# Kernel optimization log

Hardware: AMD Instinct MI355X
Metric: run time of the kernel (lower is better)

Reference implementation:

```python
import jax, jax.numpy as jnp
import numpy as np

N = 100000      # nodes (accounts)
E = 500000      # edges (transactions)
F_NODE = 128
F_EDGE = 32
HEADS = 4
C = 64          # hidden_channels per head
HC = HEADS * C  # 256
OUT = 32
BN_EPS = 1e-5
NEG_SLOPE = 0.2


def setup_inputs() -> dict:
    key = jax.random.key(0)
    ks = jax.random.split(key, 24)
    rn = lambda k, shape, s=0.05: (jax.random.normal(k, shape, jnp.float32) * s)
    inp = {
        "x": jax.random.normal(ks[0], (N, F_NODE), jnp.float32),
        "edge_index": jax.random.randint(ks[1], (2, E), 0, N, dtype=jnp.int32),
        "edge_attr": jax.random.normal(ks[2], (E, F_EDGE), jnp.float32),
        # node_proj
        "Wp": rn(ks[3], (F_NODE, C)), "bp": jnp.zeros((C,), jnp.float32),
    }
    in_dims = [C, HC, HC]
    i = 4
    for l, d in enumerate(in_dims):
        inp[f"Wg{l}"] = rn(ks[i], (d, HC)); i += 1
        inp[f"as{l}"] = rn(ks[i], (HEADS, C)); i += 1
        inp[f"ad{l}"] = rn(ks[i], (HEADS, C)); i += 1
        inp[f"bg{l}"] = jnp.zeros((HC,), jnp.float32)
        inp[f"g{l}"] = jnp.ones((HC,), jnp.float32)   # BN gamma
        inp[f"be{l}"] = jnp.zeros((HC,), jnp.float32)  # BN beta
    inp["W1"] = rn(ks[i], (2 * HC + F_EDGE, OUT)); inp["b1"] = jnp.zeros((OUT,), jnp.float32)
    inp["W2"] = rn(ks[i + 1], (OUT, 1)); inp["b2"] = jnp.zeros((1,), jnp.float32)
    return inp


def _gat_layer(h, src, dst, Wg, att_s, att_d, bg):
    # PyG GATConv (concat=True, add_self_loops=False), eval mode (no dropout).
    xh = (h @ Wg).reshape(N, HEADS, C)                      # [N,H,C]
    a_s = jnp.sum(xh * att_s, axis=-1)                      # [N,H]
    a_d = jnp.sum(xh * att_d, axis=-1)                      # [N,H]
    e = jax.nn.leaky_relu(a_s[src] + a_d[dst], NEG_SLOPE)   # [E,H]
    m = jax.lax.stop_gradient(jax.ops.segment_max(e, dst, num_segments=N))
    ex = jnp.exp(e - m[dst])
    den = jax.ops.segment_sum(ex, dst, num_segments=N)      # [N,H]
    alpha = ex / (den[dst] + 1e-16)                         # softmax over in-edges of dst
    agg = jax.ops.segment_sum(xh[src] * alpha[:, :, None], dst, num_segments=N)
    return agg.reshape(N, HC) + bg


def _forward(x, edge_index, edge_attr, Wp, bp,
             Wg0, as0, ad0, bg0, g0, be0,
             Wg1, as1, ad1, bg1, g1, be1,
             Wg2, as2, ad2, bg2, g2, be2,
             W1, b1, W2, b2):
    src, dst = edge_index[0], edge_index[1]
    h = jax.nn.relu(x @ Wp + bp)                            # [N,64]
    bn_scale = 1.0 / jnp.sqrt(jnp.float32(1.0) + BN_EPS)    # BN eval: mean=0, var=1
    layers = [(Wg0, as0, ad0, bg0, g0, be0),
              (Wg1, as1, ad1, bg1, g1, be1),
              (Wg2, as2, ad2, bg2, g2, be2)]
    for Wg, a_s, a_d, bg, g, be in layers:
        hn = _gat_layer(h, src, dst, Wg, a_s, a_d, bg)
        hn = jax.nn.relu(hn * (g * bn_scale) + be)          # BatchNorm(eval) + ReLU
        h = h + hn if h.shape == hn.shape else hn           # residual (skipped at layer 0)
    # decode_edges: MLP(src_emb || dst_emb || edge_attr) without materializing the concat:
    W1s, W1d, W1e = W1[:HC], W1[HC:2 * HC], W1[2 * HC:]
    z = jax.nn.relu((h @ W1s)[src] + (h @ W1d)[dst] + edge_attr @ W1e + b1)  # [E,32]
    return (z @ W2 + b2)[:, 0]                              # [E] fraud logits


def reference(x, edge_index, edge_attr, Wp, bp,
              Wg0, as0, ad0, bg0, g0, be0,
              Wg1, as1, ad1, bg1, g1, be1,
              Wg2, as2, ad2, bg2, g2, be2,
              W1, b1, W2, b2):
    return _forward(x, edge_index, edge_attr, Wp, bp,
                    Wg0, as0, ad0, bg0, g0, be0,
                    Wg1, as1, ad1, bg1, g1, be1,
                    Wg2, as2, ad2, bg2, g2, be2,
                    W1, b1, W2, b2)
```

## Files before the change

### kernel.cpp

```cpp
#include <hip/hip_runtime.h>
#include <hip/hip_fp16.h>

#define NN 100000
#define EE 500000
#define F_NODE 128
#define F_EDGE 32
#define HEADS 4
#define CC 64
#define HC 256
#define OUTD 32
#define NEG_SLOPE 0.2f
#define BN_SCALE 0.9999950000374997f
#define NB_SCAN 391
#define MPAD 100096

using half8 = __attribute__((ext_vector_type(8))) _Float16;
using f32x4 = __attribute__((ext_vector_type(4))) float;

typedef const __attribute__((address_space(1))) void* gas_ptr;
typedef __attribute__((address_space(3))) void* las_ptr;

template<int K, int NOUT, int MODE, int ATT>
__global__ __launch_bounds__(256, 2) void mgemm2(const __half* __restrict__ A,
                                                 const __half* __restrict__ Wt,
                                                 const float* __restrict__ bias,
                                                 __half* __restrict__ C,
                                                 const float* __restrict__ as_,
                                                 const float* __restrict__ ad_,
                                                 float* __restrict__ a_s,
                                                 float* __restrict__ a_d) {
    constexpr int BM = 128;
    constexpr int BN = (NOUT >= 128) ? 128 : 64;
    constexpr int MI = 4;
    constexpr int NI = BN / 32;
    constexpr int KS = K / 64;
    constexpr int ABYTES = BM * 128;
    constexpr int BBYTES = BN * 128;
    __shared__ char smem[2 * (ABYTES + BBYTES)];

    const int tid  = threadIdx.x;
    const int wave = tid >> 6, lane = tid & 63;
    const int wr = wave >> 1, wc = wave & 1;
    const int lrow = lane & 15, kq = lane >> 4;
    const int m0 = blockIdx.x * BM;
    const int n0 = blockIdx.y * BN;
    const int srow = tid >> 3;
    const int sunit = tid & 7;
    const int wofs = (tid & 192) * 16;

    auto stage = [&](int buf, int ks) {
        char* base = smem + buf * (ABYTES + BBYTES);
        const int kk = ks * 64;
#pragma unroll
        for (int it = 0; it < BM / 32; ++it) {
            const int r = srow + it * 32;
            const __half* src = A + (size_t)(m0 + r) * K + kk + ((sunit ^ (r & 7)) << 3);
            __builtin_amdgcn_global_load_lds((gas_ptr)src,
                (las_ptr)(base + it * 4096 + wofs), 16, 0, 0);
        }
#pragma unroll
        for (int it = 0; it < BN / 32; ++it) {
            const int r = srow + it * 32;
            const __half* src = Wt + (size_t)(n0 + r) * K + kk + ((sunit ^ (r & 7)) << 3);
            __builtin_amdgcn_global_load_lds((gas_ptr)src,
                (las_ptr)(base + ABYTES + it * 4096 + wofs), 16, 0, 0);
        }
    };

    f32x4 acc[MI][NI] = {};

    auto compute = [&](int buf) {
        const char* Ab = smem + buf * (ABYTES + BBYTES);
        const char* Bb = Ab + ABYTES;
#pragma unroll
        for (int k32 = 0; k32 < 2; ++k32) {
            const int ku = k32 * 4 + kq;
            half8 af[MI], bf[NI];
#pragma unroll
            for (int mi = 0; mi < MI; ++mi) {
                const int rr = wr * 64 + mi * 16 + lrow;
                af[mi] = *(const half8*)(Ab + rr * 128 + ((ku ^ (rr & 7)) << 4));
            }
#pragma unroll
            for (int ni = 0; ni < NI; ++ni) {
                const int rc = wc * (BN / 2) + ni * 16 + lrow;
                bf[ni] = *(const half8*)(Bb + rc * 128 + ((ku ^ (rc & 7)) << 4));
            }
#pragma unroll
            for (int mi = 0; mi < MI; ++mi)
#pragma unroll
                for (int ni = 0; ni < NI; ++ni)
                    acc[mi][ni] = __builtin_amdgcn_mfma_f32_16x16x32_f16(
                        af[mi], bf[ni], acc[mi][ni], 0, 0, 0);
        }
    };

    stage(0, 0);
    __syncthreads();
    int cur = 0;
#pragma unroll
    for (int ks = 0; ks < KS; ++ks) {
        if (ks + 1 < KS) stage(cur ^ 1, ks + 1);
        compute(cur);
        __syncthreads();
        cur ^= 1;
    }

    const int crow = kq * 4;
#pragma unroll
    for (int mi = 0; mi < MI; ++mi) {
#pragma unroll
        for (int ni = 0; ni < NI; ++ni) {
            const int col = n0 + wc * (BN / 2) + ni * 16 + lrow;
            float bcol = (MODE == 1) ? bias[col] : 0.f;
#pragma unroll
            for (int r = 0; r < 4; ++r) {
                float v = acc[mi][ni][r];
                if constexpr (MODE == 1) v = fmaxf(v + bcol, 0.f);
                const int row = m0 + wr * 64 + mi * 16 + crow + r;
                C[(size_t)row * NOUT + col] = __float2half(v);
            }
        }
    }

    if constexpr (ATT) {
        const int head = (n0 + wc * 64) >> 6;
        float wsv[NI], wdv[NI];
#pragma unroll
        for (int ni = 0; ni < NI; ++ni) {
            const int col = n0 + wc * (BN / 2) + ni * 16 + lrow;
            wsv[ni] = as_[col];
            wdv[ni] = ad_[col];
        }
#pragma unroll
        for (int mi = 0; mi < MI; ++mi) {
#pragma unroll
            for (int r = 0; r < 4; ++r) {
                float ss = 0.f, dd = 0.f;
#pragma unroll
                for (int ni = 0; ni < NI; ++ni) {
                    ss += acc[mi][ni][r] * wsv[ni];
                    dd += acc[mi][ni][r] * wdv[ni];
                }
#pragma unroll
                for (int off = 8; off >= 1; off >>= 1) {
                    ss += __shfl_xor(ss, off, 64);
                    dd += __shfl_xor(dd, off, 64);
                }
                if (lrow == 0) {
                    const int row = m0 + wr * 64 + mi * 16 + crow + r;
                    a_s[row * HEADS + head] = ss;
                    a_d[row * HEADS + head] = dd;
                }
            }
        }
    }
}

__global__ __launch_bounds__(256) void wt_conv(const float* __restrict__ W,
                                               __half* __restrict__ Wt,
                                               int K, int N) {
    int idx = blockIdx.x * 256 + threadIdx.x;
    if (idx >= K * N) return;
    int n = idx / K, k = idx % K;
    Wt[idx] = __float2half(W[k * N + n]);
}

__global__ __launch_bounds__(256) void wt_final(const float* __restrict__ W1,
                                                __half* __restrict__ Wt) {
    int idx = blockIdx.x * 256 + threadIdx.x;
    if (idx >= 64 * 256) return;
    int n = idx >> 8, k = idx & 255;
    float v = (n < 32) ? W1[k * 32 + n] : W1[(256 + k) * 32 + (n - 32)];
    Wt[idx] = __float2half(v);
}

__global__ __launch_bounds__(256) void cvt_x(const float* __restrict__ x,
                                             __half* __restrict__ x16) {
    int i = blockIdx.x * 256 + threadIdx.x;
    float4 v = ((const float4*)x)[i];
    __half2* o = (__half2*)x16 + (size_t)i * 2;
    o[0] = __floats2half2_rn(v.x, v.y);
    o[1] = __floats2half2_rn(v.z, v.w);
}

__global__ __launch_bounds__(256) void csr_count(const int* __restrict__ dst,
                                                 int* __restrict__ deg,
                                                 int* __restrict__ pos) {
    int e = blockIdx.x * 256 + threadIdx.x;
    if (e >= EE) return;
    pos[e] = atomicAdd(deg + dst[e], 1);
}

__device__ __forceinline__ int wave_incl_scan(int v, int lane) {
#pragma unroll
    for (int off = 1; off < 64; off <<= 1) {
        int t = __shfl_up(v, off, 64);
        if (lane >= off) v += t;
    }
    return v;
}

__global__ __launch_bounds__(256) void scan1(const int* __restrict__ deg,
                                             int* __restrict__ rowptr,
                                             int* __restrict__ bsum) {
    int tid = threadIdx.x, n = blockIdx.x * 256 + tid;
    int lane = tid & 63, wave = tid >> 6;
    int d = (n < NN) ? deg[n] : 0;
    int v = wave_incl_scan(d, lane);
    __shared__ int ws[4];
    if (lane == 63) ws[wave] = v;
    __syncthreads();
    int woff = 0;
    for (int w = 0; w < wave; ++w) woff += ws[w];
    int incl = v + woff;
    if (n < NN) rowptr[n] = incl - d;
    if (tid == 255) bsum[blockIdx.x] = incl;
}

__global__ __launch_bounds__(512) void scan2(const int* __restrict__ bsum,
                                             int* __restrict__ boff) {
    int t = threadIdx.x;
    int lane = t & 63, wave = t >> 6;
    int d = (t < NB_SCAN) ? bsum[t] : 0;
    int v = wave_incl_scan(d, lane);
    __shared__ int ws[8];
    if (lane == 63) ws[wave] = v;
    __syncthreads();
    int woff = 0;
    for (int w = 0; w < wave; ++w) woff += ws[w];
    if (t < NB_SCAN) boff[t] = v + woff - d;
}

__global__ __launch_bounds__(256) void scan3(int* __restrict__ rowptr,
                                             const int* __restrict__ boff) {
    int n = blockIdx.x * 256 + threadIdx.x;
    if (n == 0) rowptr[NN] = EE;
    if (n < NN) rowptr[n] += boff[blockIdx.x];
}

__global__ __launch_bounds__(256) void csr_scatter(const int* __restrict__ src,
                                                   const int* __restrict__ dst,
                                                   const int* __restrict__ rowptr,
                                                   const int* __restrict__ pos,
                                                   int* __restrict__ srcs) {
    int e = blockIdx.x * 256 + threadIdx.x;
    if (e >= EE) return;
    srcs[rowptr[dst[e]] + pos[e]] = src[e];
}

__global__ __launch_bounds__(256) void gather_agg(const int* __restrict__ rowptr,
                                                  const int* __restrict__ srcs,
                                                  const float* __restrict__ a_s,
                                                  const float* __restrict__ a_d,
                                                  const __half* __restrict__ xh,
                                                  const float* __restrict__ bg,
                                                  const float* __restrict__ g,
                                                  const float* __restrict__ be,
                                                  __half* __restrict__ h,
                                                  int residual) {
    const int n = blockIdx.x * 4 + (threadIdx.x >> 6);
    const int lane = threadIdx.x & 63;
    if (n >= NN) return;
    const int hl = lane >> 5;
    const int l5 = lane & 31;
    const int hd = l5 >> 3;
    const int c0 = l5 * 8;

    const int start = rowptr[n], end = rowptr[n + 1];
    const float adv = a_d[n * HEADS + hd];

    float acc[8] = {};
    float den = 0.f;

    for (int i = start + hl; i < end; i += 8) {
        int  j0 = i,                 j1 = (i + 2 < end) ? i + 2 : i;
        int  j2 = (i + 4 < end) ? i + 4 : i;
        int  j3 = (i + 6 < end) ? i + 6 : i;
        const int s0 = srcs[j0], s1 = srcs[j1], s2 = srcs[j2], s3 = srcs[j3];

        float v0 = a_s[s0 * HEADS + hd] + adv;
        float v1 = a_s[s1 * HEADS + hd] + adv;
        float v2 = a_s[s2 * HEADS + hd] + adv;
        float v3 = a_s[s3 * HEADS + hd] + adv;
        v0 = fmaxf(v0, v0 * NEG_SLOPE);
        v1 = fmaxf(v1, v1 * NEG_SLOPE);
        v2 = fmaxf(v2, v2 * NEG_SLOPE);
        v3 = fmaxf(v3, v3 * NEG_SLOPE);
        float e0 = __expf(v0);
        float e1 = (i + 2 < end) ? __expf(v1) : 0.f;
        float e2 = (i + 4 < end) ? __expf(v2) : 0.f;
        float e3 = (i + 6 < end) ? __expf(v3) : 0.f;

        half8 r0 = *(const half8*)(xh + (size_t)s0 * HC + c0);
        half8 r1 = *(const half8*)(xh + (size_t)s1 * HC + c0);
        half8 r2 = *(const half8*)(xh + (size_t)s2 * HC + c0);
        half8 r3 = *(const half8*)(xh + (size_t)s3 * HC + c0);

#pragma unroll
        for (int k = 0; k < 8; ++k)
            acc[k] += e0 * (float)r0[k] + e1 * (float)r1[k]
                    + e2 * (float)r2[k] + e3 * (float)r3[k];
        den += e0 + e1 + e2 + e3;
    }

    den += __shfl_xor(den, 32, 64);
#pragma unroll
    for (int k = 0; k < 8; ++k) acc[k] += __shfl_xor(acc[k], 32, 64);

    if (hl != 0) return;
    const float inv = 1.f / (den + 1e-16f);

    float bgv[8], gv[8], bev[8];
    *(float4*)(bgv)     = *(const float4*)(bg + c0);
    *(float4*)(bgv + 4) = *(const float4*)(bg + c0 + 4);
    *(float4*)(gv)      = *(const float4*)(g + c0);
    *(float4*)(gv + 4)  = *(const float4*)(g + c0 + 4);
    *(float4*)(bev)     = *(const float4*)(be + c0);
    *(float4*)(bev + 4) = *(const float4*)(be + c0 + 4);

    half8* hp = (half8*)(h + (size_t)n * HC + c0);
    float r[8];
#pragma unroll
    for (int k = 0; k < 8; ++k)
        r[k] = fmaxf((acc[k] * inv + bgv[k]) * (gv[k] * BN_SCALE) + bev[k], 0.f);
    if (residual) {
        half8 old = *hp;
#pragma unroll
        for (int k = 0; k < 8; ++k) r[k] += (float)old[k];
    }
    half8 o;
#pragma unroll
    for (int k = 0; k < 8; ++k) o[k] = (_Float16)r[k];
    __builtin_nontemporal_store(o, hp);
}

__global__ __launch_bounds__(256) void edge_final(const float* __restrict__ ea,
                                                  const __half* __restrict__ w1et,
                                                  const float* __restrict__ b1,
                                                  const int* __restrict__ src,
                                                  const int* __restrict__ dst,
                                                  const __half* __restrict__ hshd,
                                                  const float* __restrict__ W2,
                                                  const float* __restrict__ b2,
                                                  float* __restrict__ out) {
    __shared__ float zl[64][36];
    const int wave = threadIdx.x >> 6, lane = threadIdx.x & 63;
    const int e0 = blockIdx.x * 64;
    const int lrow = lane & 15, kofs = (lane >> 4) * 8;

    int er = e0 + wave * 16 + lrow;
    if (er >= EE) er = EE - 1;
    const float* ap = ea + (size_t)er * F_EDGE + kofs;
    float4 f0 = *(const float4*)ap;
    float4 f1 = *(const float4*)(ap + 4);
    half8 a;
    a[0] = (_Float16)f0.x; a[1] = (_Float16)f0.y;
    a[2] = (_Float16)f0.z; a[3] = (_Float16)f0.w;
    a[4] = (_Float16)f1.x; a[5] = (_Float16)f1.y;
    a[6] = (_Float16)f1.z; a[7] = (_Float16)f1.w;

    half8 b0 = *(const half8*)(w1et + (size_t)lrow * 32 + kofs);
    half8 b1v = *(const half8*)(w1et + (size_t)(16 + lrow) * 32 + kofs);
    f32x4 acc0 = {}, acc1 = {};
    acc0 = __builtin_amdgcn_mfma_f32_16x16x32_f16(a, b0,  acc0, 0, 0, 0);
    acc1 = __builtin_amdgcn_mfma_f32_16x16x32_f16(a, b1v, acc1, 0, 0, 0);

    const int crow = (lane >> 4) * 4;
    const float bc0 = b1[lrow], bc1 = b1[16 + lrow];
#pragma unroll
    for (int r = 0; r < 4; ++r) {
        zl[wave * 16 + crow + r][lrow]      = acc0[r] + bc0;
        zl[wave * 16 + crow + r][16 + lrow] = acc1[r] + bc1;
    }
    __syncthreads();

    const int el = threadIdx.x >> 2, j0 = (threadIdx.x & 3) * 8;
    const int e = e0 + el;
    const bool ok = e < EE;
    const int s = ok ? src[e] : 0;
    const int d = ok ? dst[e] : 0;

    half8 hs = *(const half8*)(hshd + (size_t)s * 64 + j0);
    half8 hdv = *(const half8*)(hshd + (size_t)d * 64 + 32 + j0);
    float w2v[8];
    *(float4*)(w2v)     = *(const float4*)(W2 + j0);
    *(float4*)(w2v + 4) = *(const float4*)(W2 + j0 + 4);
    float4 z0 = *(const float4*)&zl[el][j0];
    float4 z1 = *(const float4*)&zl[el][j0 + 4];

    float acc = 0.f;
    const float* zp0 = &z0.x;
    const float* zp1 = &z1.x;
#pragma unroll
    for (int i = 0; i < 4; ++i) {
        float z = zp0[i] + (float)hs[i] + (float)hdv[i];
        acc += fmaxf(z, 0.f) * w2v[i];
    }
#pragma unroll
    for (int i = 0; i < 4; ++i) {
        float z = zp1[i] + (float)hs[4 + i] + (float)hdv[4 + i];
        acc += fmaxf(z, 0.f) * w2v[4 + i];
    }
    acc += __shfl_xor(acc, 1, 64);
    acc += __shfl_xor(acc, 2, 64);
    if (ok && (threadIdx.x & 3) == 0) out[e] = acc + b2[0];
}

extern "C" void kernel_launch(void* const* d_in, const int* in_sizes, int n_in,
                              void* d_out, int out_size, void* d_ws, size_t ws_size,
                              hipStream_t stream) {
    const float* x  = (const float*)d_in[0];
    const int*   ei = (const int*)d_in[1];
    const float* ea = (const float*)d_in[2];
    const float* Wp = (const float*)d_in[3];
    const float* bp = (const float*)d_in[4];
    const float* W1 = (const float*)d_in[23];
    const float* b1 = (const float*)d_in[24];
    const float* W2 = (const float*)d_in[25];
    const float* b2 = (const float*)d_in[26];
    const int* src = ei;
    const int* dst = ei + EE;

    float* ws = (float*)d_ws;
    __half* h      = (__half*)(ws);
    __half* xh     = (__half*)(ws + 12820000);
    __half* x16    = (__half*)(ws + 25640000);
    __half* h0     = (__half*)(ws + 32050000);
    __half* hshd   = (__half*)(ws + 35260000);
    float*  a_s    = ws + 38470000;
    float*  a_d    = ws + 38880000;
    int*    rowptr = (int*)(ws + 41270000);
    int*    deg    = (int*)(ws + 41380000);
    int*    pos    = (int*)(ws + 41480000);
    int*    srcs   = (int*)(ws + 42490000);
    int*    bsum   = (int*)(ws + 42990000);
    int*    boff   = (int*)(ws + 42991000);
    __half* wpt    = (__half*)(ws + 42992000);
    __half* wgt    = (__half*)(ws + 43000000);
    __half* w1t    = (__half*)(ws + 43020000);
    float*  out    = (float*)d_out;

    const int MB = MPAD / 128;

    hipMemsetAsync(deg, 0, (size_t)NN * sizeof(int), stream);
    csr_count<<<(EE + 255) / 256, 256, 0, stream>>>(dst, deg, pos);
    scan1<<<NB_SCAN, 256, 0, stream>>>(deg, rowptr, bsum);
    scan2<<<1, 512, 0, stream>>>(bsum, boff);
    scan3<<<NB_SCAN, 256, 0, stream>>>(rowptr, boff);
    csr_scatter<<<(EE + 255) / 256, 256, 0, stream>>>(src, dst, rowptr, pos, srcs);

    cvt_x<<<NN * F_NODE / 4 / 256, 256, 0, stream>>>(x, x16);
    wt_conv<<<(F_NODE * 64 + 255) / 256, 256, 0, stream>>>(Wp, wpt, F_NODE, 64);

    mgemm2<F_NODE, 64, 1, 0><<<dim3(MB, 1), 256, 0, stream>>>(
        x16, wpt, bp, h0, nullptr, nullptr, nullptr, nullptr);

    for (int l = 0; l < 3; ++l) {
        const float* Wg  = (const float*)d_in[5 + 6 * l];
        const float* as_ = (const float*)d_in[6 + 6 * l];
        const float* ad_ = (const float*)d_in[7 + 6 * l];
        const float* bg  = (const float*)d_in[8 + 6 * l];
        const float* g   = (const float*)d_in[9 + 6 * l];
        const float* be  = (const float*)d_in[10 + 6 * l];

        if (l == 0) {
            wt_conv<<<(CC * HC + 255) / 256, 256, 0, stream>>>(Wg, wgt, CC, HC);
            mgemm2<CC, HC, 0, 1><<<dim3(MB, 2), 256, 0, stream>>>(
                h0, wgt, nullptr, xh, as_, ad_, a_s, a_d);
        } else {
            wt_conv<<<(HC * HC + 255) / 256, 256, 0, stream>>>(Wg, wgt, HC, HC);
            mgemm2<HC, HC, 0, 1><<<dim3(MB, 2), 256, 0, stream>>>(
                h, wgt, nullptr, xh, as_, ad_, a_s, a_d);
        }

        gather_agg<<<(NN + 3) / 4, 256, 0, stream>>>(rowptr, srcs, a_s, a_d, xh,
                                                     bg, g, be, h, l > 0 ? 1 : 0);
    }

    wt_final<<<(64 * 256 + 255) / 256, 256, 0, stream>>>(W1, w1t);
    mgemm2<HC, 64, 0, 0><<<dim3(MB, 1), 256, 0, stream>>>(
        h, w1t, nullptr, hshd, nullptr, nullptr, nullptr, nullptr);

    wt_conv<<<(32 * 32 + 255) / 256, 256, 0, stream>>>(W1 + 2 * HC * OUTD, wpt, 32, 32);
    edge_final<<<(EE + 63) / 64, 256, 0, stream>>>(ea, wpt, b1, src, dst, hshd, W2, b2, out);
}
```

Measured before the change: 393.8 us.

## Fuse fp32-to-fp16 input conversion into first GEMM and batch weight prep

Removes the separate cvt_x pass by having the projection GEMM load fp32 x rows into registers, convert them to fp16 and write them to swizzled LDS, with the global loads overlapped against the MFMA compute. All weight transpose/convert kernels are merged into one prep_all launch at the start. Minor gather_agg cleanups drop the bounds check and a redundant index. The intent is to save a full read-write pass over x and several small launches, at the cost of register-staged loads in the first GEMM instead of direct global-to-LDS copies.

```diff
diff --git a/kernel.cpp b/kernel.cpp
--- a/kernel.cpp
+++ b/kernel.cpp
@@ -20,7 +20,7 @@
 typedef const __attribute__((address_space(1))) void* gas_ptr;
 typedef __attribute__((address_space(3))) void* las_ptr;
 
-template<int K, int NOUT, int MODE, int ATT>
+template<int K, int NOUT, int MODE, int ATT, int AF32>
 __global__ __launch_bounds__(256, 2) void mgemm2(const __half* __restrict__ A,
                                                  const __half* __restrict__ Wt,
                                                  const float* __restrict__ bias,
@@ -28,7 +28,8 @@
                                                  const float* __restrict__ as_,
                                                  const float* __restrict__ ad_,
                                                  float* __restrict__ a_s,
-                                                 float* __restrict__ a_d) {
+                                                 float* __restrict__ a_d,
+                                                 const float* __restrict__ A32) {
     constexpr int BM = 128;
     constexpr int BN = (NOUT >= 128) ? 128 : 64;
     constexpr int MI = 4;
@@ -48,16 +49,20 @@
     const int sunit = tid & 7;
     const int wofs = (tid & 192) * 16;
 
-    auto stage = [&](int buf, int ks) {
+    auto stageA16 = [&](int buf, int ks) {
         char* base = smem + buf * (ABYTES + BBYTES);
         const int kk = ks * 64;
 #pragma unroll
-        for (int it = 0; it < BM / 32; ++it) {
+        for (int it = 0; it < 4; ++it) {
             const int r = srow + it * 32;
             const __half* src = A + (size_t)(m0 + r) * K + kk + ((sunit ^ (r & 7)) << 3);
             __builtin_amdgcn_global_load_lds((gas_ptr)src,
                 (las_ptr)(base + it * 4096 + wofs), 16, 0, 0);
         }
+    };
+    auto stageB = [&](int buf, int ks) {
+        char* base = smem + buf * (ABYTES + BBYTES);
+        const int kk = ks * 64;
 #pragma unroll
         for (int it = 0; it < BN / 32; ++it) {
             const int r = srow + it * 32;
@@ -67,6 +72,32 @@
         }
     };
 
+    float4 ar[4][2];
+    auto loadA32 = [&](int ks) {
+        const int kk = ks * 64;
+#pragma unroll
+        for (int it = 0; it < 4; ++it) {
+            int rg = m0 + srow + it * 32;
+            rg = (rg < NN) ? rg : NN - 1;
+            const float* sp = A32 + (size_t)rg * K + kk + sunit * 8;
+            ar[it][0] = *(const float4*)sp;
+            ar[it][1] = *(const float4*)(sp + 4);
+        }
+    };
+    auto writeA32 = [&](int buf) {
+        char* base = smem + buf * (ABYTES + BBYTES);
+#pragma unroll
+        for (int it = 0; it < 4; ++it) {
+            const int r = srow + it * 32;
+            half8 hv;
+            hv[0] = (_Float16)ar[it][0].x; hv[1] = (_Float16)ar[it][0].y;
+            hv[2] = (_Float16)ar[it][0].z; hv[3] = (_Float16)ar[it][0].w;
+            hv[4] = (_Float16)ar[it][1].x; hv[5] = (_Float16)ar[it][1].y;
+            hv[6] = (_Float16)ar[it][1].z; hv[7] = (_Float16)ar[it][1].w;
+            *(half8*)(base + r * 128 + ((sunit ^ (r & 7)) << 4)) = hv;
+        }
+    };
+
     f32x4 acc[MI][NI] = {};
 
     auto compute = [&](int buf) {
@@ -95,13 +126,18 @@
         }
     };
 
-    stage(0, 0);
+    if constexpr (AF32) { loadA32(0); stageB(0, 0); writeA32(0); }
+    else                { stageA16(0, 0); stageB(0, 0); }
     __syncthreads();
     int cur = 0;
 #pragma unroll
     for (int ks = 0; ks < KS; ++ks) {
-        if (ks + 1 < KS) stage(cur ^ 1, ks + 1);
+        if (ks + 1 < KS) {
+            if constexpr (AF32) { loadA32(ks + 1); stageB(cur ^ 1, ks + 1); }
+            else                { stageA16(cur ^ 1, ks + 1); stageB(cur ^ 1, ks + 1); }
+        }
         compute(cur);
+        if constexpr (AF32) { if (ks + 1 < KS) writeA32(cur ^ 1); }
         __syncthreads();
         cur ^= 1;
     }
@@ -157,31 +193,44 @@
     }
 }
 
-__global__ __launch_bounds__(256) void wt_conv(const float* __restrict__ W,
-                                               __half* __restrict__ Wt,
-                                               int K, int N) {
+#define PREP_TOTAL (8192 + 16384 + 65536 + 65536 + 16384 + 1024)
+__global__ __launch_bounds__(256) void prep_all(const float* __restrict__ Wp,
+                                                const float* __restrict__ Wg0,
+                                                const float* __restrict__ Wg1,
+                                                const float* __restrict__ Wg2,
+                                                const float* __restrict__ W1,
+                                                __half* __restrict__ wpt,
+                                                __half* __restrict__ wg0t,
+                                                __half* __restrict__ wg1t,
+                                                __half* __restrict__ wg2t,
+                                                __half* __restrict__ w1t,
+                                                __half* __restrict__ w1et) {
     int idx = blockIdx.x * 256 + threadIdx.x;
-    if (idx >= K * N) return;
-    int n = idx / K, k = idx % K;
-    Wt[idx] = __float2half(W[k * N + n]);
-}
-
-__global__ __launch_bounds__(256) void wt_final(const float* __restrict__ W1,
-                                                __half* __restrict__ Wt) {
-    int idx = blockIdx.x * 256 + threadIdx.x;
-    if (idx >= 64 * 256) return;
-    int n = idx >> 8, k = idx & 255;
-    float v = (n < 32) ? W1[k * 32 + n] : W1[(256 + k) * 32 + (n - 32)];
-    Wt[idx] = __float2half(v);
-}
-
-__global__ __launch_bounds__(256) void cvt_x(const float* __restrict__ x,
-                                             __half* __restrict__ x16) {
-    int i = blockIdx.x * 256 + threadIdx.x;
-    float4 v = ((const float4*)x)[i];
-    __half2* o = (__half2*)x16 + (size_t)i * 2;
-    o[0] = __floats2half2_rn(v.x, v.y);
-    o[1] = __floats2half2_rn(v.z, v.w);
+    if (idx < 8192) {
+        int n = idx >> 7, k = idx & 127;
+        wpt[idx] = __float2half(Wp[k * 64 + n]);
+    } else if (idx < 24576) {
+        int i = idx - 8192;
+        int n = i >> 6, k = i & 63;
+        wg0t[i] = __float2half(Wg0[k * 256 + n]);
+    } else if (idx < 90112) {
+        int i = idx - 24576;
+        int n = i >> 8, k = i & 255;
+        wg1t[i] = __float2half(Wg1[k * 256 + n]);
+    } else if (idx < 155648) {
+        int i = idx - 90112;
+        int n = i >> 8, k = i & 255;
+        wg2t[i] = __float2half(Wg2[k * 256 + n]);
+    } else if (idx < 172032) {
+        int i = idx - 155648;
+        int n = i >> 8, k = i & 255;
+        float v = (n < 32) ? W1[k * 32 + n] : W1[(256 + k) * 32 + (n - 32)];
+        w1t[i] = __float2half(v);
+    } else if (idx < PREP_TOTAL) {
+        int i = idx - 172032;
+        int n = i >> 5, k = i & 31;
+        w1et[i] = __float2half(W1[2 * HC * OUTD + k * 32 + n]);
+    }
 }
 
 __global__ __launch_bounds__(256) void csr_count(const int* __restrict__ dst,
@@ -261,7 +310,6 @@
                                                   int residual) {
     const int n = blockIdx.x * 4 + (threadIdx.x >> 6);
     const int lane = threadIdx.x & 63;
-    if (n >= NN) return;
     const int hl = lane >> 5;
     const int l5 = lane & 31;
     const int hd = l5 >> 3;
@@ -274,10 +322,10 @@
     float den = 0.f;
 
     for (int i = start + hl; i < end; i += 8) {
-        int  j0 = i,                 j1 = (i + 2 < end) ? i + 2 : i;
+        int  j1 = (i + 2 < end) ? i + 2 : i;
         int  j2 = (i + 4 < end) ? i + 4 : i;
         int  j3 = (i + 6 < end) ? i + 6 : i;
-        const int s0 = srcs[j0], s1 = srcs[j1], s2 = srcs[j2], s3 = srcs[j3];
+        const int s0 = srcs[i], s1 = srcs[j1], s2 = srcs[j2], s3 = srcs[j3];
 
         float v0 = a_s[s0 * HEADS + hd] + adv;
         float v1 = a_s[s1 * HEADS + hd] + adv;
@@ -425,7 +473,6 @@
     float* ws = (float*)d_ws;
     __half* h      = (__half*)(ws);
     __half* xh     = (__half*)(ws + 12820000);
-    __half* x16    = (__half*)(ws + 25640000);
     __half* h0     = (__half*)(ws + 32050000);
     __half* hshd   = (__half*)(ws + 35260000);
     float*  a_s    = ws + 38470000;
@@ -437,27 +484,30 @@
     int*    bsum   = (int*)(ws + 42990000);
     int*    boff   = (int*)(ws + 42991000);
     __half* wpt    = (__half*)(ws + 42992000);
-    __half* wgt    = (__half*)(ws + 43000000);
-    __half* w1t    = (__half*)(ws + 43020000);
+    __half* wg0t   = (__half*)(ws + 43000000);
+    __half* wg1t   = (__half*)(ws + 43010000);
+    __half* wg2t   = (__half*)(ws + 43045000);
+    __half* w1t    = (__half*)(ws + 43080000);
+    __half* w1et   = (__half*)(ws + 43090000);
     float*  out    = (float*)d_out;
 
     const int MB = MPAD / 128;
 
     hipMemsetAsync(deg, 0, (size_t)NN * sizeof(int), stream);
+    prep_all<<<(PREP_TOTAL + 255) / 256, 256, 0, stream>>>(
+        Wp, (const float*)d_in[5], (const float*)d_in[11], (const float*)d_in[17],
+        W1, wpt, wg0t, wg1t, wg2t, w1t, w1et);
     csr_count<<<(EE + 255) / 256, 256, 0, stream>>>(dst, deg, pos);
     scan1<<<NB_SCAN, 256, 0, stream>>>(deg, rowptr, bsum);
     scan2<<<1, 512, 0, stream>>>(bsum, boff);
     scan3<<<NB_SCAN, 256, 0, stream>>>(rowptr, boff);
     csr_scatter<<<(EE + 255) / 256, 256, 0, stream>>>(src, dst, rowptr, pos, srcs);
 
-    cvt_x<<<NN * F_NODE / 4 / 256, 256, 0, stream>>>(x, x16);
-    wt_conv<<<(F_NODE * 64 + 255) / 256, 256, 0, stream>>>(Wp, wpt, F_NODE, 64);
-
-    mgemm2<F_NODE, 64, 1, 0><<<dim3(MB, 1), 256, 0, stream>>>(
-        x16, wpt, bp, h0, nullptr, nullptr, nullptr, nullptr);
-
+    mgemm2<F_NODE, 64, 1, 0, 1><<<dim3(MB, 1), 256, 0, stream>>>(
+        nullptr, wpt, bp, h0, nullptr, nullptr, nullptr, nullptr, x);
+
+    const __half* wgt_l[3] = {wg0t, wg1t, wg2t};
     for (int l = 0; l < 3; ++l) {
-        const float* Wg  = (const float*)d_in[5 + 6 * l];
         const float* as_ = (const float*)d_in[6 + 6 * l];
         const float* ad_ = (const float*)d_in[7 + 6 * l];
         const float* bg  = (const float*)d_in[8 + 6 * l];
@@ -465,23 +515,20 @@
         const float* be  = (const float*)d_in[10 + 6 * l];
 
         if (l == 0) {
-            wt_conv<<<(CC * HC + 255) / 256, 256, 0, stream>>>(Wg, wgt, CC, HC);
-            mgemm2<CC, HC, 0, 1><<<dim3(MB, 2), 256, 0, stream>>>(
-                h0, wgt, nullptr, xh, as_, ad_, a_s, a_d);
+            mgemm2<CC, HC, 0, 1, 0><<<dim3(MB, 2), 256, 0, stream>>>(
+                h0, wgt_l[0], nullptr, xh, as_, ad_, a_s, a_d, nullptr);
         } else {
-            wt_conv<<<(HC * HC + 255) / 256, 256, 0, stream>>>(Wg, wgt, HC, HC);
-            mgemm2<HC, HC, 0, 1><<<dim3(MB, 2), 256, 0, stream>>>(
-                h, wgt, nullptr, xh, as_, ad_, a_s, a_d);
-        }
-
-        gather_agg<<<(NN + 3) / 4, 256, 0, stream>>>(rowptr, srcs, a_s, a_d, xh,
-                                                     bg, g, be, h, l > 0 ? 1 : 0);
-    }
-
-    wt_final<<<(64 * 256 + 255) / 256, 256, 0, stream>>>(W1, w1t);
-    mgemm2<HC, 64, 0, 0><<<dim3(MB, 1), 256, 0, stream>>>(
-        h, w1t, nullptr, hshd, nullptr, nullptr, nullptr, nullptr);
-
-    wt_conv<<<(32 * 32 + 255) / 256, 256, 0, stream>>>(W1 + 2 * HC * OUTD, wpt, 32, 32);
-    edge_final<<<(EE + 63) / 64, 256, 0, stream>>>(ea, wpt, b1, src, dst, hshd, W2, b2, out);
-}
+            mgemm2<HC, HC, 0, 1, 0><<<dim3(MB, 2), 256, 0, stream>>>(
+                h, wgt_l[l], nullptr, xh, as_, ad_, a_s, a_d, nullptr);
+        }
+
+        gather_agg<<<NN / 4, 256, 0, stream>>>(rowptr, srcs, a_s, a_d, xh,
+                                               bg, g, be, h, l > 0 ? 1 : 0);
+    }
+
+    mgemm2<HC, 64, 0, 0, 0><<<dim3(MB, 1), 256, 0, stream>>>(
+        h, w1t, nullptr, hshd, nullptr, nullptr, nullptr, nullptr, nullptr);
+
+    edge_final<<<(EE + 63) / 64, 256, 0, stream>>>(ea, w1et, b1, src, dst,
+                                                   hshd, W2, b2, out);
+}
```

Result: faster. 374.3 us (-5.0%).
